# Kernel optimization log

Measured on AMD Instinct MI355X. Metric: run time of the kernel, lower is better.

## Reference

```python
import jax, jax.numpy as jnp
import numpy as np

N_NODES = 20000


def _gcn_conv(x, edge_index, W, b):
    """PyG GCNConv: add self-loops, symmetric normalization, x @ W, scatter-add, + bias."""
    n = x.shape[0]
    loops = jnp.arange(n, dtype=edge_index.dtype)
    src = jnp.concatenate([edge_index[0], loops])  # [E+N]
    dst = jnp.concatenate([edge_index[1], loops])  # [E+N]
    # degree of target nodes (edge weight 1), self-loops guarantee deg >= 1
    deg = jax.ops.segment_sum(jnp.ones_like(dst, dtype=x.dtype), dst, num_segments=n)
    dinv = jax.lax.rsqrt(deg)
    norm = dinv[src] * dinv[dst]  # [E+N]
    h = x @ W  # [n, out] dense GEMM before aggregation (standard GCNConv ordering)
    msg = h[src] * norm[:, None]  # gather + scale over edges
    out = jax.ops.segment_sum(msg, dst, num_segments=n)  # scatter-add to targets
    return out + b


def setup_inputs() -> dict:
    key = jax.random.key(0)
    k = jax.random.split(key, 6)
    in_f, h_f, n_cls = 512, 512, 256
    x = jax.random.normal(k[0], (N_NODES, in_f), dtype=jnp.float32)
    edge_index = jax.random.randint(k[1], (2, 160000), 0, N_NODES, dtype=jnp.int64)
    W1 = jax.random.normal(k[2], (in_f, h_f), dtype=jnp.float32) * (1.0 / np.sqrt(in_f))
    b1 = jnp.zeros((h_f,), dtype=jnp.float32)
    W2 = jax.random.normal(k[3], (h_f, n_cls), dtype=jnp.float32) * (1.0 / np.sqrt(h_f))
    b2 = jnp.zeros((n_cls,), dtype=jnp.float32)
    return {"x": x, "edge_index": edge_index, "W1": W1, "b1": b1, "W2": W2, "b2": b2}


def reference(x, edge_index, W1, b1, W2, b2):
    h = jax.nn.relu(_gcn_conv(x, edge_index, W1, b1))
    h = jax.nn.relu(_gcn_conv(h, edge_index, W2, b2))
    # F.dropout in eval mode is identity; reference is deterministic eval-mode forward
    return h
```

## Files before the change

### kernel.cpp

```cpp
#include <hip/hip_runtime.h>


typedef __bf16 bf16x8 __attribute__((ext_vector_type(8)));
typedef float floatx4 __attribute__((ext_vector_type(4)));
typedef unsigned short ushort_t;
typedef unsigned int uint_t;

__device__ inline ushort_t f2bf(float f) {
    unsigned u = __builtin_bit_cast(unsigned, f);
    unsigned r = (u + 0x7FFFu + ((u >> 16) & 1u)) >> 16;
    return (ushort_t)r;
}
__device__ inline float bf_lo(uint_t u) { return __builtin_bit_cast(float, u << 16); }
__device__ inline float bf_hi(uint_t u) { return __builtin_bit_cast(float, u & 0xFFFF0000u); }

__device__ inline void transpose_tile(const float* __restrict__ in,
                                      ushort_t* __restrict__ out,
                                      int K, int N, int k0, int n0,
                                      ushort_t (*tile)[33]) {
    int tx = threadIdx.x & 31, ty = threadIdx.x >> 5;
    for (int r = ty; r < 32; r += 8)
        tile[r][tx] = f2bf(in[(size_t)(k0 + r) * N + n0 + tx]);
    __syncthreads();
    for (int r = ty; r < 32; r += 8)
        out[(size_t)(n0 + r) * K + k0 + tx] = tile[tx][r];
}

__global__ __launch_bounds__(256) void prep_fused(
    const int* __restrict__ dst, int* __restrict__ deg, int e, int nb_e,
    const float* __restrict__ x, ushort_t* __restrict__ xb, long xcount, int nb_conv,
    const float* __restrict__ W1, ushort_t* __restrict__ w1t,
    const float* __restrict__ W2, ushort_t* __restrict__ w2t) {
    __shared__ ushort_t tile[32][33];
    int b = blockIdx.x;
    if (b < nb_e) {
        int i = b * 256 + threadIdx.x;
        if (i < e) atomicAdd(&deg[dst[i]], 1);
        return;
    }
    b -= nb_e;
    if (b < nb_conv) {
        long i = ((long)b * 256 + threadIdx.x) * 4;
        if (i < xcount) {
            float4 v = *(const float4*)(x + i);
            ushort4 o = make_ushort4(f2bf(v.x), f2bf(v.y), f2bf(v.z), f2bf(v.w));
            *(ushort4*)(xb + i) = o;
        }
        return;
    }
    b -= nb_conv;
    if (b < 256) {
        transpose_tile(W1, w1t, 512, 512, (b >> 4) * 32, (b & 15) * 32, tile);
        return;
    }
    b -= 256;
    transpose_tile(W2, w2t, 512, 256, (b >> 3) * 32, (b & 7) * 32, tile);
}

__global__ __launch_bounds__(256) void assign_ranges(const int* __restrict__ deg,
                                                     int* counter,
                                                     int* __restrict__ row_start,
                                                     int* __restrict__ fill_pos,
                                                     float* __restrict__ dinv, int n) {
    __shared__ int sd[256];
    __shared__ int sbase;
    int t = threadIdx.x;
    int i = blockIdx.x * 256 + t;
    int v = (i < n) ? deg[i] : 0;
    if (i < n) dinv[i] = 1.0f / sqrtf((float)(v + 1));
    sd[t] = v;
    __syncthreads();
    for (int o = 1; o < 256; o <<= 1) {
        int a = (t >= o) ? sd[t - o] : 0;
        __syncthreads();
        sd[t] += a;
        __syncthreads();
    }
    if (t == 255) sbase = atomicAdd(counter, sd[255]);
    __syncthreads();
    if (i < n) {
        int s = sbase + sd[t] - v;
        row_start[i] = s;
        fill_pos[i] = s;
    }
}

__global__ __launch_bounds__(256) void fill_csr(const int* __restrict__ src,
                                                const int* __restrict__ dst,
                                                int* __restrict__ fill_pos,
                                                int* __restrict__ col, int e) {
    int i = blockIdx.x * 256 + threadIdx.x;
    if (i < e) {
        int p = atomicAdd(&fill_pos[dst[i]], 1);
        col[p] = src[i];
    }
}

__global__ __launch_bounds__(256) void gemm_mfma(const ushort_t* __restrict__ A,
                                                 const ushort_t* __restrict__ BT,
                                                 const float* __restrict__ dinv,
                                                 ushort_t* __restrict__ C,
                                                 int M, int N, int K) {
    __shared__ __align__(16) ushort_t As[4096];
    __shared__ __align__(16) ushort_t Bs[4096];
    const int tid = threadIdx.x;
    const int w = tid >> 6, lane = tid & 63;
    const int q = lane >> 4, ml = lane & 15;
    const int wm = (w >> 1) * 64, wn = (w & 1) * 64;
    const int row0 = blockIdx.y * 128, col0 = blockIdx.x * 128;

    const int off0 = w * 1024 + lane * 16;
    const int off1 = off0 + 4096;
    auto srcA = [&](int off) -> const ushort_t* {
        int r = off >> 6, s = (off >> 4) & 3, qq = s ^ ((r >> 1) & 3);
        int gr = min(row0 + r, M - 1);
        return A + (size_t)gr * K + qq * 8;
    };
    auto srcB = [&](int off) -> const ushort_t* {
        int r = off >> 6, s = (off >> 4) & 3, qq = s ^ ((r >> 1) & 3);
        return BT + (size_t)(col0 + r) * K + qq * 8;
    };
    const ushort_t* ga0 = srcA(off0);
    const ushort_t* ga1 = srcA(off1);
    const ushort_t* gb0 = srcB(off0);
    const ushort_t* gb1 = srcB(off1);
    ushort_t* lA0 = As + w * 512;
    ushort_t* lA1 = As + 2048 + w * 512;
    ushort_t* lB0 = Bs + w * 512;
    ushort_t* lB1 = Bs + 2048 + w * 512;

    const int selA = (ml >> 1) & 3;
    int aoff[4], boff[4];
#pragma unroll
    for (int i = 0; i < 4; i++) {
        aoff[i] = (wm + i * 16 + ml) * 32 + ((q ^ selA) << 3);
        boff[i] = (wn + i * 16 + ml) * 32 + ((q ^ selA) << 3);
    }

    floatx4 acc[4][4];
#pragma unroll
    for (int i = 0; i < 4; i++)
#pragma unroll
        for (int j = 0; j < 4; j++) acc[i][j] = (floatx4)0.0f;

    for (int kt = 0; kt < K; kt += 32) {
        __builtin_amdgcn_global_load_lds(
            (const __attribute__((address_space(1))) unsigned*)ga0,
            (__attribute__((address_space(3))) unsigned*)lA0, 16, 0, 0);
        __builtin_amdgcn_global_load_lds(
            (const __attribute__((address_space(1))) unsigned*)ga1,
            (__attribute__((address_space(3))) unsigned*)lA1, 16, 0, 0);
        __builtin_amdgcn_global_load_lds(
            (const __attribute__((address_space(1))) unsigned*)gb0,
            (__attribute__((address_space(3))) unsigned*)lB0, 16, 0, 0);
        __builtin_amdgcn_global_load_lds(
            (const __attribute__((address_space(1))) unsigned*)gb1,
            (__attribute__((address_space(3))) unsigned*)lB1, 16, 0, 0);
        ga0 += 32; ga1 += 32; gb0 += 32; gb1 += 32;
        __syncthreads();

        bf16x8 af[4], bfr[4];
#pragma unroll
        for (int i = 0; i < 4; i++) {
            af[i] = *(const bf16x8*)(As + aoff[i]);
            bfr[i] = *(const bf16x8*)(Bs + boff[i]);
        }
#pragma unroll
        for (int i = 0; i < 4; i++)
#pragma unroll
            for (int j = 0; j < 4; j++)
                acc[i][j] = __builtin_amdgcn_mfma_f32_16x16x32_bf16(af[i], bfr[j], acc[i][j], 0, 0, 0);
        __syncthreads();
    }

#pragma unroll
    for (int i = 0; i < 4; i++) {
        int rbase = row0 + wm + i * 16 + q * 4;
        float pd[4];
#pragma unroll
        for (int r = 0; r < 4; r++) pd[r] = (rbase + r < M) ? dinv[rbase + r] : 0.0f;
#pragma unroll
        for (int j = 0; j < 4; j++) {
            int gc = col0 + wn + j * 16 + ml;
#pragma unroll
            for (int r = 0; r < 4; r++) {
                int gr = rbase + r;
                if (gr < M) C[(size_t)gr * N + gc] = f2bf(pd[r] * acc[i][j][r]);
            }
        }
    }
}

__global__ __launch_bounds__(256) void aggregate1(const uint_t* __restrict__ g,
                                                  const int* __restrict__ row_start,
                                                  const int* __restrict__ deg,
                                                  const int* __restrict__ col_idx,
                                                  const float* __restrict__ dinv,
                                                  const float* __restrict__ bias,
                                                  uint_t* __restrict__ out) {
    const int d = blockIdx.x, t = threadIdx.x;
    const int s0 = row_start[d], cnt = deg[d];
    const float pd = dinv[d];
    const size_t base = (size_t)d * 256 + t;

    uint_t us = g[base];
    float acc0 = bf_lo(us), acc1 = bf_hi(us);

    int e = 0;
    for (; e + 8 <= cnt; e += 8) {
        uint_t u[8];
#pragma unroll
        for (int j = 0; j < 8; j++)
            u[j] = g[(size_t)col_idx[s0 + e + j] * 256 + t];
#pragma unroll
        for (int j = 0; j < 8; j++) { acc0 += bf_lo(u[j]); acc1 += bf_hi(u[j]); }
    }
    if (e + 4 <= cnt) {
        uint_t u[4];
#pragma unroll
        for (int j = 0; j < 4; j++)
            u[j] = g[(size_t)col_idx[s0 + e + j] * 256 + t];
#pragma unroll
        for (int j = 0; j < 4; j++) { acc0 += bf_lo(u[j]); acc1 += bf_hi(u[j]); }
        e += 4;
    }
    for (; e < cnt; e++) {
        uint_t u = g[(size_t)col_idx[s0 + e] * 256 + t];
        acc0 += bf_lo(u);
        acc1 += bf_hi(u);
    }
    float2 b = *(const float2*)(bias + t * 2);
    float o0 = fmaxf(fmaf(pd, acc0, b.x), 0.0f);
    float o1 = fmaxf(fmaf(pd, acc1, b.y), 0.0f);
    out[base] = (uint_t)f2bf(o0) | ((uint_t)f2bf(o1) << 16);
}

__global__ __launch_bounds__(128) void aggregate2(const uint_t* __restrict__ g,
                                                  const int* __restrict__ row_start,
                                                  const int* __restrict__ deg,
                                                  const int* __restrict__ col_idx,
                                                  const float* __restrict__ dinv,
                                                  const float* __restrict__ bias,
                                                  float* __restrict__ out) {
    const int d = blockIdx.x, t = threadIdx.x;
    const int s0 = row_start[d], cnt = deg[d];
    const float pd = dinv[d];
    const size_t base = (size_t)d * 128 + t;

    uint_t us = g[base];
    float acc0 = bf_lo(us), acc1 = bf_hi(us);

    int e = 0;
    for (; e + 8 <= cnt; e += 8) {
        uint_t u[8];
#pragma unroll
        for (int j = 0; j < 8; j++)
            u[j] = g[(size_t)col_idx[s0 + e + j] * 128 + t];
#pragma unroll
        for (int j = 0; j < 8; j++) { acc0 += bf_lo(u[j]); acc1 += bf_hi(u[j]); }
    }
    if (e + 4 <= cnt) {
        uint_t u[4];
#pragma unroll
        for (int j = 0; j < 4; j++)
            u[j] = g[(size_t)col_idx[s0 + e + j] * 128 + t];
#pragma unroll
        for (int j = 0; j < 4; j++) { acc0 += bf_lo(u[j]); acc1 += bf_hi(u[j]); }
        e += 4;
    }
    for (; e < cnt; e++) {
        uint_t u = g[(size_t)col_idx[s0 + e] * 128 + t];
        acc0 += bf_lo(u);
        acc1 += bf_hi(u);
    }
    float2 b = *(const float2*)(bias + t * 2);
    float2 o;
    o.x = fmaxf(fmaf(pd, acc0, b.x), 0.0f);
    o.y = fmaxf(fmaf(pd, acc1, b.y), 0.0f);
    *(float2*)(out + (size_t)d * 256 + t * 2) = o;
}

extern "C" void kernel_launch(void* const* d_in, const int* in_sizes, int n_in,
                              void* d_out, int out_size, void* d_ws, size_t ws_size,
                              hipStream_t stream) {
    const float* x  = (const float*)d_in[0];
    const int*   ei = (const int*)d_in[1];
    const float* W1 = (const float*)d_in[2];
    const float* b1 = (const float*)d_in[3];
    const float* W2 = (const float*)d_in[4];
    const float* b2 = (const float*)d_in[5];
    float* out = (float*)d_out;

    const int FIN = 512, FH = 512, FOUT = 256;
    const int n = in_sizes[0] / FIN;
    const int e = in_sizes[1] / 2;
    const int* src = ei;
    const int* dst = ei + e;

    auto align_up = [](size_t v) { return (v + 255) & ~(size_t)255; };
    char* w = (char*)d_ws;
    int*      deg       = (int*)w;
    int*      counter   = deg + n;
    w += align_up((size_t)(n + 1) * 4);
    float*    dinv      = (float*)w;    w += align_up((size_t)n * 4);
    int*      row_start = (int*)w;      w += align_up((size_t)n * 4);
    int*      fill_pos  = (int*)w;      w += align_up((size_t)n * 4);
    int*      col_idx   = (int*)w;      w += align_up((size_t)e * 4);
    ushort_t* xb        = (ushort_t*)w; w += align_up((size_t)n * FIN * 2);
    ushort_t* w1t       = (ushort_t*)w; w += align_up((size_t)FH * FIN * 2);
    ushort_t* w2t       = (ushort_t*)w; w += align_up((size_t)FOUT * FH * 2);
    ushort_t* g         = (ushort_t*)w; w += align_up((size_t)n * FH * 2);
    ushort_t* h1b       = (ushort_t*)w; w += align_up((size_t)n * FH * 2);

    const int nb_n = (n + 255) / 256;
    const int nb_e = (e + 255) / 256;
    const long xcount = (long)n * FIN;
    const int nb_conv = (int)((xcount / 4 + 255) / 256);

    hipMemsetAsync(deg, 0, (size_t)(n + 1) * 4, stream);

    prep_fused<<<nb_e + nb_conv + 256 + 128, 256, 0, stream>>>(
        dst, deg, e, nb_e, x, xb, xcount, nb_conv, W1, w1t, W2, w2t);
    assign_ranges<<<nb_n, 256, 0, stream>>>(deg, counter, row_start, fill_pos, dinv, n);
    fill_csr<<<nb_e, 256, 0, stream>>>(src, dst, fill_pos, col_idx, e);

    const int mb = (n + 127) / 128;
    gemm_mfma<<<dim3(FH / 128, mb), 256, 0, stream>>>(xb, w1t, dinv, g, n, FH, FIN);
    aggregate1<<<n, 256, 0, stream>>>((const uint_t*)g, row_start, deg, col_idx, dinv, b1, (uint_t*)h1b);
    gemm_mfma<<<dim3(FOUT / 128, mb), 256, 0, stream>>>(h1b, w2t, dinv, g, n, FOUT, FH);
    aggregate2<<<n, 128, 0, stream>>>((const uint_t*)g, row_start, deg, col_idx, dinv, b2, out);

    (void)ws_size; (void)n_in; (void)out_size;
}
```

Measured before the change: 217.7 us.

## Fuse degree scan into first GEMM and widen aggregation loads with shuffled indices

The assign_ranges scan now runs as extra blocks of the first GEMM launch. That GEMM no longer pre-scales rows by dinv, so it does not depend on the degrees. Layer-1 aggregation instead applies the per-source dinv inside the gather, and only layer 2 keeps row scaling in the GEMM. Both aggregation kernels now load uint2 (4 bf16) per thread with half the threads, and each 8-edge batch reads its column indices once and broadcasts them via __shfl. This cuts a launch, overlaps the scan with the GEMM, and widens memory transactions, at the cost of an extra dinv gather per edge in layer 1.

```diff
diff --git a/kernel.cpp b/kernel.cpp
--- a/kernel.cpp
+++ b/kernel.cpp
@@ -57,34 +57,6 @@
     transpose_tile(W2, w2t, 512, 256, (b >> 3) * 32, (b & 7) * 32, tile);
 }
 
-__global__ __launch_bounds__(256) void assign_ranges(const int* __restrict__ deg,
-                                                     int* counter,
-                                                     int* __restrict__ row_start,
-                                                     int* __restrict__ fill_pos,
-                                                     float* __restrict__ dinv, int n) {
-    __shared__ int sd[256];
-    __shared__ int sbase;
-    int t = threadIdx.x;
-    int i = blockIdx.x * 256 + t;
-    int v = (i < n) ? deg[i] : 0;
-    if (i < n) dinv[i] = 1.0f / sqrtf((float)(v + 1));
-    sd[t] = v;
-    __syncthreads();
-    for (int o = 1; o < 256; o <<= 1) {
-        int a = (t >= o) ? sd[t - o] : 0;
-        __syncthreads();
-        sd[t] += a;
-        __syncthreads();
-    }
-    if (t == 255) sbase = atomicAdd(counter, sd[255]);
-    __syncthreads();
-    if (i < n) {
-        int s = sbase + sd[t] - v;
-        row_start[i] = s;
-        fill_pos[i] = s;
-    }
-}
-
 __global__ __launch_bounds__(256) void fill_csr(const int* __restrict__ src,
                                                 const int* __restrict__ dst,
                                                 int* __restrict__ fill_pos,
@@ -96,18 +68,46 @@
     }
 }
 
-__global__ __launch_bounds__(256) void gemm_mfma(const ushort_t* __restrict__ A,
-                                                 const ushort_t* __restrict__ BT,
-                                                 const float* __restrict__ dinv,
-                                                 ushort_t* __restrict__ C,
-                                                 int M, int N, int K) {
+__global__ __launch_bounds__(256) void gemm_mfma(
+    const ushort_t* __restrict__ A, const ushort_t* __restrict__ BT,
+    const float* __restrict__ dinv, ushort_t* __restrict__ C,
+    int M, int N, int K, int nbx, int gemm_blocks, int scale,
+    const int* __restrict__ deg, int* counter, int* __restrict__ row_start,
+    int* __restrict__ fill_pos, float* __restrict__ dinv_out, int n) {
     __shared__ __align__(16) ushort_t As[4096];
     __shared__ __align__(16) ushort_t Bs[4096];
+    __shared__ int sd[256];
+    __shared__ int sbase;
+
+    if ((int)blockIdx.x >= gemm_blocks) {
+        int t = threadIdx.x;
+        int i = ((int)blockIdx.x - gemm_blocks) * 256 + t;
+        int v = (i < n) ? deg[i] : 0;
+        if (i < n) dinv_out[i] = 1.0f / sqrtf((float)(v + 1));
+        sd[t] = v;
+        __syncthreads();
+        for (int o = 1; o < 256; o <<= 1) {
+            int a = (t >= o) ? sd[t - o] : 0;
+            __syncthreads();
+            sd[t] += a;
+            __syncthreads();
+        }
+        if (t == 255) sbase = atomicAdd(counter, sd[255]);
+        __syncthreads();
+        if (i < n) {
+            int s = sbase + sd[t] - v;
+            row_start[i] = s;
+            fill_pos[i] = s;
+        }
+        return;
+    }
+
+    const int bx = (int)blockIdx.x % nbx, by = (int)blockIdx.x / nbx;
     const int tid = threadIdx.x;
     const int w = tid >> 6, lane = tid & 63;
     const int q = lane >> 4, ml = lane & 15;
     const int wm = (w >> 1) * 64, wn = (w & 1) * 64;
-    const int row0 = blockIdx.y * 128, col0 = blockIdx.x * 128;
+    const int row0 = by * 128, col0 = bx * 128;
 
     const int off0 = w * 1024 + lane * 16;
     const int off1 = off0 + 4096;
@@ -178,7 +178,8 @@
         int rbase = row0 + wm + i * 16 + q * 4;
         float pd[4];
 #pragma unroll
-        for (int r = 0; r < 4; r++) pd[r] = (rbase + r < M) ? dinv[rbase + r] : 0.0f;
+        for (int r = 0; r < 4; r++)
+            pd[r] = (scale && rbase + r < M) ? dinv[rbase + r] : 1.0f;
 #pragma unroll
         for (int j = 0; j < 4; j++) {
             int gc = col0 + wn + j * 16 + ml;
@@ -191,93 +192,105 @@
     }
 }
 
-__global__ __launch_bounds__(256) void aggregate1(const uint_t* __restrict__ g,
+__global__ __launch_bounds__(128) void aggregate1(const uint2* __restrict__ g,
                                                   const int* __restrict__ row_start,
                                                   const int* __restrict__ deg,
                                                   const int* __restrict__ col_idx,
                                                   const float* __restrict__ dinv,
                                                   const float* __restrict__ bias,
-                                                  uint_t* __restrict__ out) {
-    const int d = blockIdx.x, t = threadIdx.x;
-    const int s0 = row_start[d], cnt = deg[d];
-    const float pd = dinv[d];
-    const size_t base = (size_t)d * 256 + t;
-
-    uint_t us = g[base];
-    float acc0 = bf_lo(us), acc1 = bf_hi(us);
-
-    int e = 0;
-    for (; e + 8 <= cnt; e += 8) {
-        uint_t u[8];
-#pragma unroll
-        for (int j = 0; j < 8; j++)
-            u[j] = g[(size_t)col_idx[s0 + e + j] * 256 + t];
-#pragma unroll
-        for (int j = 0; j < 8; j++) { acc0 += bf_lo(u[j]); acc1 += bf_hi(u[j]); }
-    }
-    if (e + 4 <= cnt) {
-        uint_t u[4];
-#pragma unroll
-        for (int j = 0; j < 4; j++)
-            u[j] = g[(size_t)col_idx[s0 + e + j] * 256 + t];
-#pragma unroll
-        for (int j = 0; j < 4; j++) { acc0 += bf_lo(u[j]); acc1 += bf_hi(u[j]); }
-        e += 4;
-    }
-    for (; e < cnt; e++) {
-        uint_t u = g[(size_t)col_idx[s0 + e] * 256 + t];
-        acc0 += bf_lo(u);
-        acc1 += bf_hi(u);
-    }
-    float2 b = *(const float2*)(bias + t * 2);
-    float o0 = fmaxf(fmaf(pd, acc0, b.x), 0.0f);
-    float o1 = fmaxf(fmaf(pd, acc1, b.y), 0.0f);
-    out[base] = (uint_t)f2bf(o0) | ((uint_t)f2bf(o1) << 16);
-}
-
-__global__ __launch_bounds__(128) void aggregate2(const uint_t* __restrict__ g,
-                                                  const int* __restrict__ row_start,
-                                                  const int* __restrict__ deg,
-                                                  const int* __restrict__ col_idx,
-                                                  const float* __restrict__ dinv,
-                                                  const float* __restrict__ bias,
-                                                  float* __restrict__ out) {
+                                                  uint2* __restrict__ out) {
     const int d = blockIdx.x, t = threadIdx.x;
     const int s0 = row_start[d], cnt = deg[d];
     const float pd = dinv[d];
     const size_t base = (size_t)d * 128 + t;
 
-    uint_t us = g[base];
-    float acc0 = bf_lo(us), acc1 = bf_hi(us);
+    uint2 us = g[base];
+    float a0 = pd * bf_lo(us.x), a1 = pd * bf_hi(us.x);
+    float a2 = pd * bf_lo(us.y), a3 = pd * bf_hi(us.y);
 
     int e = 0;
     for (; e + 8 <= cnt; e += 8) {
-        uint_t u[8];
-#pragma unroll
-        for (int j = 0; j < 8; j++)
-            u[j] = g[(size_t)col_idx[s0 + e + j] * 128 + t];
-#pragma unroll
-        for (int j = 0; j < 8; j++) { acc0 += bf_lo(u[j]); acc1 += bf_hi(u[j]); }
-    }
-    if (e + 4 <= cnt) {
-        uint_t u[4];
-#pragma unroll
-        for (int j = 0; j < 4; j++)
-            u[j] = g[(size_t)col_idx[s0 + e + j] * 128 + t];
-#pragma unroll
-        for (int j = 0; j < 4; j++) { acc0 += bf_lo(u[j]); acc1 += bf_hi(u[j]); }
-        e += 4;
+        int cv = col_idx[s0 + e + (t & 7)];
+        float dv = dinv[cv];
+        uint2 u[8];
+        float ps[8];
+#pragma unroll
+        for (int j = 0; j < 8; j++) {
+            int s = __shfl(cv, j);
+            ps[j] = __shfl(dv, j);
+            u[j] = g[(size_t)s * 128 + t];
+        }
+#pragma unroll
+        for (int j = 0; j < 8; j++) {
+            a0 = fmaf(ps[j], bf_lo(u[j].x), a0);
+            a1 = fmaf(ps[j], bf_hi(u[j].x), a1);
+            a2 = fmaf(ps[j], bf_lo(u[j].y), a2);
+            a3 = fmaf(ps[j], bf_hi(u[j].y), a3);
+        }
     }
     for (; e < cnt; e++) {
-        uint_t u = g[(size_t)col_idx[s0 + e] * 128 + t];
-        acc0 += bf_lo(u);
-        acc1 += bf_hi(u);
-    }
-    float2 b = *(const float2*)(bias + t * 2);
-    float2 o;
-    o.x = fmaxf(fmaf(pd, acc0, b.x), 0.0f);
-    o.y = fmaxf(fmaf(pd, acc1, b.y), 0.0f);
-    *(float2*)(out + (size_t)d * 256 + t * 2) = o;
+        int s = col_idx[s0 + e];
+        float ps = dinv[s];
+        uint2 u = g[(size_t)s * 128 + t];
+        a0 = fmaf(ps, bf_lo(u.x), a0);
+        a1 = fmaf(ps, bf_hi(u.x), a1);
+        a2 = fmaf(ps, bf_lo(u.y), a2);
+        a3 = fmaf(ps, bf_hi(u.y), a3);
+    }
+    float4 b = *(const float4*)(bias + t * 4);
+    float o0 = fmaxf(fmaf(pd, a0, b.x), 0.0f);
+    float o1 = fmaxf(fmaf(pd, a1, b.y), 0.0f);
+    float o2 = fmaxf(fmaf(pd, a2, b.z), 0.0f);
+    float o3 = fmaxf(fmaf(pd, a3, b.w), 0.0f);
+    uint2 o;
+    o.x = (uint_t)f2bf(o0) | ((uint_t)f2bf(o1) << 16);
+    o.y = (uint_t)f2bf(o2) | ((uint_t)f2bf(o3) << 16);
+    out[base] = o;
+}
+
+__global__ __launch_bounds__(64) void aggregate2(const uint2* __restrict__ g,
+                                                 const int* __restrict__ row_start,
+                                                 const int* __restrict__ deg,
+                                                 const int* __restrict__ col_idx,
+                                                 const float* __restrict__ dinv,
+                                                 const float* __restrict__ bias,
+                                                 float* __restrict__ out) {
+    const int d = blockIdx.x, t = threadIdx.x;
+    const int s0 = row_start[d], cnt = deg[d];
+    const float pd = dinv[d];
+    const size_t base = (size_t)d * 64 + t;
+
+    uint2 us = g[base];
+    float a0 = bf_lo(us.x), a1 = bf_hi(us.x);
+    float a2 = bf_lo(us.y), a3 = bf_hi(us.y);
+
+    int e = 0;
+    for (; e + 8 <= cnt; e += 8) {
+        int cv = col_idx[s0 + e + (t & 7)];
+        uint2 u[8];
+#pragma unroll
+        for (int j = 0; j < 8; j++) {
+            int s = __shfl(cv, j);
+            u[j] = g[(size_t)s * 64 + t];
+        }
+#pragma unroll
+        for (int j = 0; j < 8; j++) {
+            a0 += bf_lo(u[j].x); a1 += bf_hi(u[j].x);
+            a2 += bf_lo(u[j].y); a3 += bf_hi(u[j].y);
+        }
+    }
+    for (; e < cnt; e++) {
+        uint2 u = g[(size_t)col_idx[s0 + e] * 64 + t];
+        a0 += bf_lo(u.x); a1 += bf_hi(u.x);
+        a2 += bf_lo(u.y); a3 += bf_hi(u.y);
+    }
+    float4 b = *(const float4*)(bias + t * 4);
+    float4 o;
+    o.x = fmaxf(fmaf(pd, a0, b.x), 0.0f);
+    o.y = fmaxf(fmaf(pd, a1, b.y), 0.0f);
+    o.z = fmaxf(fmaf(pd, a2, b.z), 0.0f);
+    o.w = fmaxf(fmaf(pd, a3, b.w), 0.0f);
+    *(float4*)(out + (size_t)d * 256 + t * 4) = o;
 }
 
 extern "C" void kernel_launch(void* const* d_in, const int* in_sizes, int n_in,
@@ -321,14 +334,25 @@
 
     prep_fused<<<nb_e + nb_conv + 256 + 128, 256, 0, stream>>>(
         dst, deg, e, nb_e, x, xb, xcount, nb_conv, W1, w1t, W2, w2t);
-    assign_ranges<<<nb_n, 256, 0, stream>>>(deg, counter, row_start, fill_pos, dinv, n);
+
+    const int mb = (n + 127) / 128;
+    {
+        int gemm_blocks = (FH / 128) * mb;
+        gemm_mfma<<<gemm_blocks + nb_n, 256, 0, stream>>>(
+            xb, w1t, nullptr, g, n, FH, FIN, FH / 128, gemm_blocks, 0,
+            deg, counter, row_start, fill_pos, dinv, n);
+    }
     fill_csr<<<nb_e, 256, 0, stream>>>(src, dst, fill_pos, col_idx, e);
-
-    const int mb = (n + 127) / 128;
-    gemm_mfma<<<dim3(FH / 128, mb), 256, 0, stream>>>(xb, w1t, dinv, g, n, FH, FIN);
-    aggregate1<<<n, 256, 0, stream>>>((const uint_t*)g, row_start, deg, col_idx, dinv, b1, (uint_t*)h1b);
-    gemm_mfma<<<dim3(FOUT / 128, mb), 256, 0, stream>>>(h1b, w2t, dinv, g, n, FOUT, FH);
-    aggregate2<<<n, 128, 0, stream>>>((const uint_t*)g, row_start, deg, col_idx, dinv, b2, out);
+    aggregate1<<<n, 128, 0, stream>>>((const uint2*)g, row_start, deg, col_idx,
+                                      dinv, b1, (uint2*)h1b);
+    {
+        int gemm_blocks = (FOUT / 128) * mb;
+        gemm_mfma<<<gemm_blocks, 256, 0, stream>>>(
+            h1b, w2t, dinv, g, n, FOUT, FH, FOUT / 128, gemm_blocks, 1,
+            nullptr, nullptr, nullptr, nullptr, nullptr, 0);
+    }
+    aggregate2<<<n, 64, 0, stream>>>((const uint2*)g, row_start, deg, col_idx,
+                                     dinv, b2, out);
 
     (void)ws_size; (void)n_in; (void)out_size;
 }
```

New measurement: 210.9 us. 1.03x faster.
